# Performance work log

Hardware: AMD Instinct MI355X
Metric: run time of the kernel (lower is better)

Reference implementation:

```python
import jax, jax.numpy as jnp
import numpy as np

GROUPS = 8
EPS = 1e-5


def setup_inputs() -> dict:
    key = jax.random.key(0)
    ks = jax.random.split(key, 7)
    b, c, h, w = 32, 256, 32, 32
    x = jax.random.normal(ks[0], (b, c, h, w), dtype=jnp.float32)
    gn_weight = jax.random.normal(ks[1], (c,), dtype=jnp.float32) * 0.02 + 1.0
    gn_bias = jax.random.normal(ks[2], (c,), dtype=jnp.float32) * 0.02
    w_qkv = jax.random.normal(ks[3], (3 * c, c), dtype=jnp.float32) / np.sqrt(c)
    b_qkv = jax.random.normal(ks[4], (3 * c,), dtype=jnp.float32) * 0.01
    w_out = jax.random.normal(ks[5], (c, c), dtype=jnp.float32) / np.sqrt(c)
    b_out = jax.random.normal(ks[6], (c,), dtype=jnp.float32) * 0.01
    return {"x": x, "gn_weight": gn_weight, "gn_bias": gn_bias,
            "w_qkv": w_qkv, "b_qkv": b_qkv, "w_out": w_out, "b_out": b_out}


def group_norm(x, weight, bias):
    b, c, h, w = x.shape
    xg = x.reshape(b, GROUPS, c // GROUPS, h, w)
    mean = jnp.mean(xg, axis=(2, 3, 4), keepdims=True)
    var = jnp.var(xg, axis=(2, 3, 4), keepdims=True)
    xg = (xg - mean) * jax.lax.rsqrt(var + EPS)
    x = xg.reshape(b, c, h, w)
    return x * weight[None, :, None, None] + bias[None, :, None, None]


def reference(x, gn_weight, gn_bias, w_qkv, b_qkv, w_out, b_out):
    b, c, h, w = x.shape
    x_norm = group_norm(x, gn_weight, gn_bias)
    # 1x1 conv == channel matmul: (b, 3c, h, w)
    qkv = jnp.einsum('oc,bchw->bohw', w_qkv, x_norm) + b_qkv[None, :, None, None]
    q, k, v = jnp.split(qkv, 3, axis=1)
    hw = h * w
    q = q.reshape(b, c, hw)  # used transposed: (b, hw, c)
    k = k.reshape(b, c, hw)
    v = v.reshape(b, c, hw)
    scale = 1.0 / jnp.sqrt(jnp.float32(c))
    attn = jax.nn.softmax(jnp.einsum('bcs,bct->bst', q, k) * scale, axis=-1)  # (b, hw, hw)
    out = jnp.einsum('bst,bct->bcs', attn, v).reshape(b, c, h, w)
    out = jnp.einsum('oc,bchw->bohw', w_out, out) + b_out[None, :, None, None]
    return out + x
```

## Files before the change

### kernel.cpp

```cpp
#include <hip/hip_runtime.h>
#include <hip/hip_bf16.h>


typedef __bf16 bf16x8 __attribute__((ext_vector_type(8)));
typedef __bf16 bf16x4 __attribute__((ext_vector_type(4)));
typedef __bf16 bf16x2 __attribute__((ext_vector_type(2)));
typedef float f32x4 __attribute__((ext_vector_type(4)));
typedef float f32x16 __attribute__((ext_vector_type(16)));

#define MFMA16(a, b, c) __builtin_amdgcn_mfma_f32_16x16x32_bf16(a, b, c, 0, 0, 0)
#define MFMA32(a, b, c) __builtin_amdgcn_mfma_f32_32x32x16_bf16(a, b, c, 0, 0, 0)

__global__ __launch_bounds__(512) void gn_kernel(const float* __restrict__ x,
                                                 const float* __restrict__ gw,
                                                 const float* __restrict__ gb,
                                                 __bf16* __restrict__ xnT,
                                                 const float* __restrict__ wqkv,
                                                 const float* __restrict__ wout,
                                                 __bf16* __restrict__ wbf) {
    __shared__ float red[16];
    __shared__ float stats[2];
    __shared__ __bf16 Lds[512][40];
    const int b = blockIdx.x >> 3, g = blockIdx.x & 7;
    const size_t base = ((size_t)b * 256 + g * 32) * 1024;
    const float* xp = x + base;
    const int t = threadIdx.x;

    {
        int widx = (blockIdx.x * 512 + t) * 2;
        const float* wsrc = (widx < 196608) ? (wqkv + widx) : (wout + (widx - 196608));
        float2 wv = *(const float2*)wsrc;
        bf16x2 wo;
        wo[0] = (__bf16)wv.x; wo[1] = (__bf16)wv.y;
        *(bf16x2*)&wbf[widx] = wo;
    }

    float s = 0.f, s2 = 0.f;
    #pragma unroll
    for (int i = 0; i < 8; i++) {
        int j = i * 512 + t;
        float4 v0 = *(const float4*)(xp + (size_t)j * 8);
        float4 v1 = *(const float4*)(xp + (size_t)j * 8 + 4);
        s  += v0.x + v0.y + v0.z + v0.w + v1.x + v1.y + v1.z + v1.w;
        s2 += v0.x*v0.x + v0.y*v0.y + v0.z*v0.z + v0.w*v0.w
            + v1.x*v1.x + v1.y*v1.y + v1.z*v1.z + v1.w*v1.w;
    }
    #pragma unroll
    for (int o = 32; o > 0; o >>= 1) { s += __shfl_down(s, o, 64); s2 += __shfl_down(s2, o, 64); }
    const int wv = t >> 6;
    if ((t & 63) == 0) { red[wv * 2] = s; red[wv * 2 + 1] = s2; }
    __syncthreads();
    if (t == 0) {
        float ts = 0.f, ts2 = 0.f;
        for (int w = 0; w < 8; w++) { ts += red[w * 2]; ts2 += red[w * 2 + 1]; }
        float mean = ts / 32768.f;
        float var = ts2 / 32768.f - mean * mean;
        stats[0] = mean; stats[1] = rsqrtf(var + 1e-5f);
    }
    __syncthreads();
    const float mean = stats[0], inv = stats[1];

    const int c = t >> 4;
    const int so = (t & 15) * 2;
    const float ga = gw[g * 32 + c], be = gb[g * 32 + c];

    for (int chunk = 0; chunk < 1024; chunk += 512) {
        #pragma unroll
        for (int i = 0; i < 16; i++) {
            int sl = so + i * 32;
            float2 v = *(const float2*)(xp + (size_t)c * 1024 + chunk + sl);
            Lds[sl][c]     = (__bf16)((v.x - mean) * inv * ga + be);
            Lds[sl + 1][c] = (__bf16)((v.y - mean) * inv * ga + be);
        }
        __syncthreads();
        {
            int sl = t;
            #pragma unroll
            for (int u = 0; u < 4; u++) {
                bf16x8 vv = *(const bf16x8*)&Lds[sl][u * 8];
                *(bf16x8*)&xnT[((size_t)b * 1024 + chunk + sl) * 256 + g * 32 + u * 8] = vv;
            }
        }
        __syncthreads();
    }
}

#define GEMM64_BODY(ArowBase_, BrowBase_)                                               \
    f32x4 acc[4][4] = {};                                                               \
    const int r_ = t >> 1, kc_ = (t & 1) * 32;                                          \
    bf16x8 pa[4], pb[4];                                                                \
    _Pragma("unroll")                                                                   \
    for (int u = 0; u < 4; u++) {                                                       \
        pa[u] = *(const bf16x8*)&(ArowBase_)[(size_t)r_ * 256 + kc_ + u * 8];           \
        pb[u] = *(const bf16x8*)&(BrowBase_)[(size_t)r_ * 256 + kc_ + u * 8];           \
    }                                                                                   \
    for (int kk = 0; kk < 256; kk += 64) {                                              \
        _Pragma("unroll")                                                               \
        for (int u = 0; u < 4; u++) {                                                   \
            *(bf16x8*)&As[r_][kc_ + u * 8] = pa[u];                                     \
            *(bf16x8*)&Bs[r_][kc_ + u * 8] = pb[u];                                     \
        }                                                                               \
        __syncthreads();                                                                \
        if (kk < 192) {                                                                 \
            _Pragma("unroll")                                                           \
            for (int u = 0; u < 4; u++) {                                               \
                pa[u] = *(const bf16x8*)&(ArowBase_)[(size_t)r_ * 256 + kk + 64 + kc_ + u * 8]; \
                pb[u] = *(const bf16x8*)&(BrowBase_)[(size_t)r_ * 256 + kk + 64 + kc_ + u * 8]; \
            }                                                                           \
        }                                                                               \
        _Pragma("unroll")                                                               \
        for (int kh = 0; kh < 2; kh++) {                                                \
            bf16x8 af[4], bfv[4];                                                       \
            _Pragma("unroll")                                                           \
            for (int im = 0; im < 4; im++)                                              \
                af[im] = *(const bf16x8*)&As[wm + im * 16 + l16][kh * 32 + quad * 8];   \
            _Pragma("unroll")                                                           \
            for (int in = 0; in < 4; in++)                                              \
                bfv[in] = *(const bf16x8*)&Bs[wn + in * 16 + l16][kh * 32 + quad * 8];  \
            _Pragma("unroll")                                                           \
            for (int im = 0; im < 4; im++)                                              \
                _Pragma("unroll")                                                       \
                for (int in = 0; in < 4; in++)                                          \
                    acc[im][in] = MFMA16(af[im], bfv[in], acc[im][in]);                 \
        }                                                                               \
        __syncthreads();                                                                \
    }

__global__ __launch_bounds__(256) void qkv_gemm(const __bf16* __restrict__ wbf,
                                                const float* __restrict__ bias,
                                                const __bf16* __restrict__ xnT,
                                                __bf16* __restrict__ qtr,
                                                __bf16* __restrict__ ktr,
                                                __bf16* __restrict__ vbuf) {
    __shared__ union {
        struct { __bf16 A[128][72]; __bf16 B[128][72]; } g;
        __bf16 ct[128][136];
    } sm;
    const int b = blockIdx.z;
    const int n0 = blockIdx.x * 128, m0 = blockIdx.y * 128;
    const int t = threadIdx.x;
    const int wave = t >> 6, lane = t & 63, quad = lane >> 4, l16 = lane & 15;
    const int wm = (wave & 1) * 64, wn = (wave >> 1) * 64;
    const __bf16* arow = wbf + (size_t)m0 * 256;
    const __bf16* brow = xnT + ((size_t)b * 1024 + n0) * 256;
    auto As = sm.g.A;
    auto Bs = sm.g.B;

    GEMM64_BODY(arow, brow)

    if (m0 < 512) {
        #pragma unroll
        for (int im = 0; im < 4; im++) {
            #pragma unroll
            for (int in = 0; in < 4; in++) {
                int ob = m0 + wm + im * 16 + quad * 4;
                bf16x4 ov;
                #pragma unroll
                for (int r = 0; r < 4; r++) ov[r] = (__bf16)(acc[im][in][r] + bias[ob + r]);
                *(bf16x4*)&sm.ct[wn + in * 16 + l16][wm + im * 16 + quad * 4] = ov;
            }
        }
        __syncthreads();
        {
            const int rbase = t >> 2, cf = t & 3;
            #pragma unroll
            for (int rr = 0; rr < 2; rr++) {
                int row = rbase + rr * 64;
                int sg = n0 + row;
                __bf16* dst = (m0 < 256) ? &qtr[((size_t)b * 1024 + sg) * 256 + m0]
                                         : &ktr[((size_t)b * 1024 + sg) * 256 + (m0 - 256)];
                #pragma unroll
                for (int u = 0; u < 4; u++) {
                    int colb = cf * 8 + u * 32;
                    *(bf16x8*)&dst[colb] = *(const bf16x8*)&sm.ct[row][colb];
                }
            }
        }
    } else {
        #pragma unroll
        for (int im = 0; im < 4; im++) {
            #pragma unroll
            for (int in = 0; in < 4; in++) {
                int cl = wm + im * 16 + quad * 4;
                int tl = wn + in * 16 + l16;
                #pragma unroll
                for (int r = 0; r < 4; r++)
                    sm.ct[cl + r][tl] = (__bf16)(acc[im][in][r] + bias[m0 + cl + r]);
            }
        }
        __syncthreads();
        {
            const int row = t >> 1, tc = (t & 1) * 64;
            const int cglob = m0 - 512 + row;
            __bf16* dst = &vbuf[((size_t)b * 256 + cglob) * 1024 + n0 + tc];
            #pragma unroll
            for (int u = 0; u < 8; u++)
                *(bf16x8*)&dst[u * 8] = *(const bf16x8*)&sm.ct[row][tc + u * 8];
        }
    }
}

__global__ __launch_bounds__(512, 2) void attn_kernel(const __bf16* __restrict__ qtr,
                                                      const __bf16* __restrict__ ktr,
                                                      const __bf16* __restrict__ vbuf,
                                                      __bf16* __restrict__ aoT) {
    __shared__ __bf16 Kt[2][32][260];
    __shared__ __bf16 Vs[2][256][36];
    __shared__ bf16x8 Pl[4][2][2][64];
    __shared__ float Lred[4][2][32];
    const int b = blockIdx.x;
    const int tid = threadIdx.x;
    const int wave = tid >> 6, lane = tid & 63, half = lane >> 5, l31 = lane & 31;
    const int pair = wave & 3, th = wave >> 2;
    const int s0 = blockIdx.y * 128 + pair * 32;
    const float kscale = 0.09016844f;

    bf16x8 aq[16];
    #pragma unroll
    for (int ks = 0; ks < 16; ks++)
        aq[ks] = *(const bf16x8*)&qtr[((size_t)b * 1024 + s0 + l31) * 256 + ks * 16 + half * 8];

    const int k_row = tid >> 3;
    const int k_cb  = (tid & 7) * 8;
    const int v_c   = tid >> 1;
    const int v_th  = tid & 1;
    const size_t kbase = (size_t)b * 1024 * 256;
    const size_t vbase = (size_t)b * 256 * 1024;

    float l_acc = 0.f;
    f32x16 o_acc[4] = {};

    bf16x8 kpre[4], vpre[4];
    #pragma unroll
    for (int u = 0; u < 4; u++) {
        kpre[u] = *(const bf16x8*)&ktr[kbase + (size_t)k_row * 256 + k_cb + u * 64];
        vpre[u] = *(const bf16x8*)&vbuf[vbase + (size_t)v_c * 1024 + v_th * 32 + u * 8];
    }

    for (int it = 0; it < 16; it++) {
        #pragma unroll
        for (int u = 0; u < 4; u++)
            *(bf16x8*)&Kt[k_row >> 5][k_row & 31][k_cb + u * 64] = kpre[u];
        #pragma unroll
        for (int u = 0; u < 4; u++) {
            const bf16x4* hv = (const bf16x4*)&vpre[u];
            const int sbase = (u >> 1) * 16 + (u & 1) * 4;
            *(bf16x4*)&Vs[v_th][v_c][sbase]     = hv[0];
            *(bf16x4*)&Vs[v_th][v_c][sbase + 8] = hv[1];
        }
        __syncthreads();
        if (it < 15) {
            const int t1 = (it + 1) * 64;
            #pragma unroll
            for (int u = 0; u < 4; u++) {
                kpre[u] = *(const bf16x8*)&ktr[kbase + (size_t)(t1 + k_row) * 256 + k_cb + u * 64];
                vpre[u] = *(const bf16x8*)&vbuf[vbase + (size_t)v_c * 1024 + t1 + v_th * 32 + u * 8];
            }
        }

        f32x16 sc_a = {}, sc_b = {};
        __builtin_amdgcn_s_setprio(1);
        #pragma unroll
        for (int ks = 0; ks < 8; ks++) {
            bf16x8 bk0 = *(const bf16x8*)&Kt[th][l31][ks * 16 + half * 8];
            bf16x8 bk1 = *(const bf16x8*)&Kt[th][l31][(ks + 8) * 16 + half * 8];
            sc_a = MFMA32(bk0, aq[ks], sc_a);
            sc_b = MFMA32(bk1, aq[ks + 8], sc_b);
        }
        __builtin_amdgcn_s_setprio(0);

        bf16x8 pf0, pf1;
        #pragma unroll
        for (int r = 0; r < 8; r++) {
            float p = exp2f((sc_a[r] + sc_b[r]) * kscale);
            l_acc += p;
            pf0[r] = (__bf16)p;
        }
        #pragma unroll
        for (int r = 8; r < 16; r++) {
            float p = exp2f((sc_a[r] + sc_b[r]) * kscale);
            l_acc += p;
            pf1[r - 8] = (__bf16)p;
        }
        Pl[pair][th][0][lane] = pf0;
        Pl[pair][th][1][lane] = pf1;
        __syncthreads();
        bf16x8 pp0 = Pl[pair][1 - th][0][lane];
        bf16x8 pp1 = Pl[pair][1 - th][1][lane];

        bf16x8 ap[4];
        if (th == 0) { ap[0] = pf0; ap[1] = pf1; ap[2] = pp0; ap[3] = pp1; }
        else         { ap[0] = pp0; ap[1] = pp1; ap[2] = pf0; ap[3] = pf1; }

        __builtin_amdgcn_s_setprio(1);
        #pragma unroll
        for (int n = 0; n < 4; n++) {
            int c = th * 128 + n * 32 + l31;
            #pragma unroll
            for (int kc = 0; kc < 4; kc++) {
                bf16x8 bv = *(const bf16x8*)&Vs[kc >> 1][c][(kc & 1) * 16 + half * 8];
                o_acc[n] = MFMA32(ap[kc], bv, o_acc[n]);
            }
        }
        __builtin_amdgcn_s_setprio(0);
        __syncthreads();
    }

    l_acc += __shfl_xor(l_acc, 32, 64);
    if (lane < 32) Lred[pair][th][l31] = l_acc;
    __syncthreads();
    #pragma unroll
    for (int r = 0; r < 16; r++) {
        int row = (r & 3) + 8 * (r >> 2) + 4 * half;
        float rinv = 1.0f / (Lred[pair][0][row] + Lred[pair][1][row]);
        #pragma unroll
        for (int n = 0; n < 4; n++) {
            int c = th * 128 + n * 32 + l31;
            aoT[((size_t)b * 1024 + s0 + row) * 256 + c] = (__bf16)(o_acc[n][r] * rinv);
        }
    }
}

__global__ __launch_bounds__(256) void proj_gemm(const __bf16* __restrict__ wbf_out,
                                                 const float* __restrict__ bias,
                                                 const __bf16* __restrict__ aoT,
                                                 const float* __restrict__ resid,
                                                 float* __restrict__ Out) {
    __shared__ union {
        struct { __bf16 A[128][72]; __bf16 B[128][72]; } g;
        float cf[64][132];
    } sm;
    const int b = blockIdx.z;
    const int n0 = blockIdx.x * 128, m0 = blockIdx.y * 128;
    const int t = threadIdx.x;
    const int wave = t >> 6, lane = t & 63, quad = lane >> 4, l16 = lane & 15;
    const int wm = (wave & 1) * 64, wn = (wave >> 1) * 64;
    const __bf16* arow = wbf_out + (size_t)m0 * 256;
    const __bf16* brow = aoT + ((size_t)b * 1024 + n0) * 256;
    auto As = sm.g.A;
    auto Bs = sm.g.B;

    GEMM64_BODY(arow, brow)

    for (int h = 0; h < 2; h++) {
        if ((wave & 1) == h) {
            #pragma unroll
            for (int im = 0; im < 4; im++)
                #pragma unroll
                for (int in = 0; in < 4; in++)
                    #pragma unroll
                    for (int r = 0; r < 4; r++)
                        sm.cf[im * 16 + quad * 4 + r][wn + in * 16 + l16] = acc[im][in][r];
        }
        __syncthreads();
        {
            const int rloc = t >> 2, cq = (t & 3) * 4;
            const int o = m0 + h * 64 + rloc;
            const float bo = bias[o];
            const float* rrow = &resid[((size_t)b * 256 + o) * 1024 + n0];
            float* orow = &Out[((size_t)b * 256 + o) * 1024 + n0];
            #pragma unroll
            for (int u = 0; u < 8; u++) {
                int col = cq + u * 16;
                f32x4 cv = *(const f32x4*)&sm.cf[rloc][col];
                float4 rv = *(const float4*)&rrow[col];
                float4 ov;
                ov.x = cv[0] + bo + rv.x;
                ov.y = cv[1] + bo + rv.y;
                ov.z = cv[2] + bo + rv.z;
                ov.w = cv[3] + bo + rv.w;
                *(float4*)&orow[col] = ov;
            }
        }
        __syncthreads();
    }
}

extern "C" void kernel_launch(void* const* d_in, const int* in_sizes, int n_in,
                              void* d_out, int out_size, void* d_ws, size_t ws_size,
                              hipStream_t stream) {
    const float* x    = (const float*)d_in[0];
    const float* gw   = (const float*)d_in[1];
    const float* gb   = (const float*)d_in[2];
    const float* wqkv = (const float*)d_in[3];
    const float* bqkv = (const float*)d_in[4];
    const float* wout = (const float*)d_in[5];
    const float* bout = (const float*)d_in[6];
    float* out = (float*)d_out;

    const size_t T16 = (size_t)32 * 1024 * 256;
    __bf16* xnT  = (__bf16*)d_ws;
    __bf16* qtr  = xnT + T16;
    __bf16* ktr  = qtr + T16;
    __bf16* vbuf = ktr + T16;
    __bf16* aoT  = vbuf + T16;
    __bf16* wbf  = aoT + T16;

    gn_kernel<<<dim3(256), 512, 0, stream>>>(x, gw, gb, xnT, wqkv, wout, wbf);
    qkv_gemm<<<dim3(8, 6, 32), 256, 0, stream>>>(wbf, bqkv, xnT, qtr, ktr, vbuf);
    attn_kernel<<<dim3(32, 8), 512, 0, stream>>>(qtr, ktr, vbuf, aoT);
    proj_gemm<<<dim3(8, 2, 32), 256, 0, stream>>>(wbf + 196608, bout, aoT, x, out);
}
```

Measured before the change: 192.1 us.

## Double-buffer K/V tiles in LDS in attention kernel to drop a barrier

Doubles the shared-memory K and V staging buffers so the next tile is written to the alternate buffer while the current one is consumed. This removes the per-iteration barrier between staging and compute, and prefetches global loads two tiles ahead. The cost is roughly doubled LDS usage, which may cut resident blocks per CU and lower occupancy.

```diff
diff --git a/kernel.cpp b/kernel.cpp
--- a/kernel.cpp
+++ b/kernel.cpp
@@ -204,8 +204,8 @@
                                                       const __bf16* __restrict__ ktr,
                                                       const __bf16* __restrict__ vbuf,
                                                       __bf16* __restrict__ aoT) {
-    __shared__ __bf16 Kt[2][32][260];
-    __shared__ __bf16 Vs[2][256][36];
+    __shared__ __bf16 Kt[2][2][32][260];
+    __shared__ __bf16 Vs[2][2][256][36];
     __shared__ bf16x8 Pl[4][2][2][64];
     __shared__ float Lred[4][2][32];
     const int b = blockIdx.x;
@@ -229,41 +229,43 @@
 
     float l_acc = 0.f;
     f32x16 o_acc[4] = {};
-
     bf16x8 kpre[4], vpre[4];
-    #pragma unroll
-    for (int u = 0; u < 4; u++) {
-        kpre[u] = *(const bf16x8*)&ktr[kbase + (size_t)k_row * 256 + k_cb + u * 64];
-        vpre[u] = *(const bf16x8*)&vbuf[vbase + (size_t)v_c * 1024 + v_th * 32 + u * 8];
-    }
+
+#define LOAD_KV(T_)                                                                           \
+    _Pragma("unroll")                                                                         \
+    for (int u = 0; u < 4; u++) {                                                             \
+        kpre[u] = *(const bf16x8*)&ktr[kbase + (size_t)((T_) + k_row) * 256 + k_cb + u * 64]; \
+        vpre[u] = *(const bf16x8*)&vbuf[vbase + (size_t)v_c * 1024 + (T_) + v_th * 32 + u * 8]; \
+    }
+
+#define STAGE_KV(bb_)                                                                         \
+    _Pragma("unroll")                                                                         \
+    for (int u = 0; u < 4; u++)                                                               \
+        *(bf16x8*)&Kt[bb_][k_row >> 5][k_row & 31][k_cb + u * 64] = kpre[u];                  \
+    _Pragma("unroll")                                                                         \
+    for (int u = 0; u < 4; u++) {                                                             \
+        const bf16x4* hv = (const bf16x4*)&vpre[u];                                           \
+        const int sbase = (u >> 1) * 16 + (u & 1) * 4;                                        \
+        *(bf16x4*)&Vs[bb_][v_th][v_c][sbase]     = hv[0];                                     \
+        *(bf16x4*)&Vs[bb_][v_th][v_c][sbase + 8] = hv[1];                                     \
+    }
+
+    LOAD_KV(0)
+    STAGE_KV(0)
+    LOAD_KV(64)
+    __syncthreads();
 
     for (int it = 0; it < 16; it++) {
-        #pragma unroll
-        for (int u = 0; u < 4; u++)
-            *(bf16x8*)&Kt[k_row >> 5][k_row & 31][k_cb + u * 64] = kpre[u];
-        #pragma unroll
-        for (int u = 0; u < 4; u++) {
-            const bf16x4* hv = (const bf16x4*)&vpre[u];
-            const int sbase = (u >> 1) * 16 + (u & 1) * 4;
-            *(bf16x4*)&Vs[v_th][v_c][sbase]     = hv[0];
-            *(bf16x4*)&Vs[v_th][v_c][sbase + 8] = hv[1];
-        }
-        __syncthreads();
-        if (it < 15) {
-            const int t1 = (it + 1) * 64;
-            #pragma unroll
-            for (int u = 0; u < 4; u++) {
-                kpre[u] = *(const bf16x8*)&ktr[kbase + (size_t)(t1 + k_row) * 256 + k_cb + u * 64];
-                vpre[u] = *(const bf16x8*)&vbuf[vbase + (size_t)v_c * 1024 + t1 + v_th * 32 + u * 8];
-            }
-        }
+        const int cur = it & 1;
+        if (it < 15) { STAGE_KV(cur ^ 1) }
+        if (it < 14) { LOAD_KV((it + 2) * 64) }
 
         f32x16 sc_a = {}, sc_b = {};
         __builtin_amdgcn_s_setprio(1);
         #pragma unroll
         for (int ks = 0; ks < 8; ks++) {
-            bf16x8 bk0 = *(const bf16x8*)&Kt[th][l31][ks * 16 + half * 8];
-            bf16x8 bk1 = *(const bf16x8*)&Kt[th][l31][(ks + 8) * 16 + half * 8];
+            bf16x8 bk0 = *(const bf16x8*)&Kt[cur][th][l31][ks * 16 + half * 8];
+            bf16x8 bk1 = *(const bf16x8*)&Kt[cur][th][l31][(ks + 8) * 16 + half * 8];
             sc_a = MFMA32(bk0, aq[ks], sc_a);
             sc_b = MFMA32(bk1, aq[ks + 8], sc_b);
         }
@@ -298,13 +300,15 @@
             int c = th * 128 + n * 32 + l31;
             #pragma unroll
             for (int kc = 0; kc < 4; kc++) {
-                bf16x8 bv = *(const bf16x8*)&Vs[kc >> 1][c][(kc & 1) * 16 + half * 8];
+                bf16x8 bv = *(const bf16x8*)&Vs[cur][kc >> 1][c][(kc & 1) * 16 + half * 8];
                 o_acc[n] = MFMA32(ap[kc], bv, o_acc[n]);
             }
         }
         __builtin_amdgcn_s_setprio(0);
         __syncthreads();
     }
+#undef LOAD_KV
+#undef STAGE_KV
 
     l_acc += __shfl_xor(l_acc, 32, 64);
     if (lane < 32) Lred[pair][th][l31] = l_acc;
```

Measured after the change: 195.9 us. Within noise of the previous version (+2.0%).

## Load GEMM tiles directly into LDS with global_load_lds and XOR swizzle

Applied to the files above, without the earlier changes.

Replaces the register-staged global-to-LDS copy in the QKV and output projection GEMMs with direct global_load_lds transfers of 16 bytes per lane. The padded LDS rows become unpadded and use an XOR swizzle on the 8-element column chunk to avoid bank conflicts. The aim is to cut VGPR pressure and the extra LDS store instructions. In exchange it drops the register prefetch of the next K slice, so loads are no longer overlapped with the MFMA work.

```diff
diff --git a/kernel.cpp b/kernel.cpp
--- a/kernel.cpp
+++ b/kernel.cpp
@@ -10,6 +10,10 @@
 
 #define MFMA16(a, b, c) __builtin_amdgcn_mfma_f32_16x16x32_bf16(a, b, c, 0, 0, 0)
 #define MFMA32(a, b, c) __builtin_amdgcn_mfma_f32_32x32x16_bf16(a, b, c, 0, 0, 0)
+
+#define GLD16(gsrc_, ldst_)                                                                  \
+    __builtin_amdgcn_global_load_lds((const __attribute__((address_space(1))) void*)(gsrc_), \
+                                     (__attribute__((address_space(3))) void*)(ldst_), 16, 0, 0)
 
 __global__ __launch_bounds__(512) void gn_kernel(const float* __restrict__ x,
                                                  const float* __restrict__ gw,
@@ -85,38 +89,31 @@
     }
 }
 
-#define GEMM64_BODY(ArowBase_, BrowBase_)                                               \
+#define GEMM64G_BODY(ArowBase_, BrowBase_)                                              \
     f32x4 acc[4][4] = {};                                                               \
-    const int r_ = t >> 1, kc_ = (t & 1) * 32;                                          \
-    bf16x8 pa[4], pb[4];                                                                \
-    _Pragma("unroll")                                                                   \
-    for (int u = 0; u < 4; u++) {                                                       \
-        pa[u] = *(const bf16x8*)&(ArowBase_)[(size_t)r_ * 256 + kc_ + u * 8];           \
-        pb[u] = *(const bf16x8*)&(BrowBase_)[(size_t)r_ * 256 + kc_ + u * 8];           \
-    }                                                                                   \
     for (int kk = 0; kk < 256; kk += 64) {                                              \
         _Pragma("unroll")                                                               \
-        for (int u = 0; u < 4; u++) {                                                   \
-            *(bf16x8*)&As[r_][kc_ + u * 8] = pa[u];                                     \
-            *(bf16x8*)&Bs[r_][kc_ + u * 8] = pb[u];                                     \
+        for (int i = 0; i < 4; i++) {                                                   \
+            const int ch = wave * 4 + i;                                                \
+            const int r = ch * 8 + (lane >> 3);                                         \
+            const int sw = ((lane & 7) ^ (r & 7)) * 8;                                  \
+            GLD16((ArowBase_) + (size_t)r * 256 + kk + sw, (char*)&As[0][0] + ch * 1024); \
+            GLD16((BrowBase_) + (size_t)r * 256 + kk + sw, (char*)&Bs[0][0] + ch * 1024); \
         }                                                                               \
         __syncthreads();                                                                \
-        if (kk < 192) {                                                                 \
-            _Pragma("unroll")                                                           \
-            for (int u = 0; u < 4; u++) {                                               \
-                pa[u] = *(const bf16x8*)&(ArowBase_)[(size_t)r_ * 256 + kk + 64 + kc_ + u * 8]; \
-                pb[u] = *(const bf16x8*)&(BrowBase_)[(size_t)r_ * 256 + kk + 64 + kc_ + u * 8]; \
-            }                                                                           \
-        }                                                                               \
         _Pragma("unroll")                                                               \
         for (int kh = 0; kh < 2; kh++) {                                                \
             bf16x8 af[4], bfv[4];                                                       \
             _Pragma("unroll")                                                           \
-            for (int im = 0; im < 4; im++)                                              \
-                af[im] = *(const bf16x8*)&As[wm + im * 16 + l16][kh * 32 + quad * 8];   \
+            for (int im = 0; im < 4; im++) {                                            \
+                const int row = wm + im * 16 + l16;                                     \
+                af[im] = *(const bf16x8*)&As[row][(((kh * 4 + quad) ^ (row & 7)) * 8)]; \
+            }                                                                           \
             _Pragma("unroll")                                                           \
-            for (int in = 0; in < 4; in++)                                              \
-                bfv[in] = *(const bf16x8*)&Bs[wn + in * 16 + l16][kh * 32 + quad * 8];  \
+            for (int in = 0; in < 4; in++) {                                            \
+                const int row = wn + in * 16 + l16;                                     \
+                bfv[in] = *(const bf16x8*)&Bs[row][(((kh * 4 + quad) ^ (row & 7)) * 8)]; \
+            }                                                                           \
             _Pragma("unroll")                                                           \
             for (int im = 0; im < 4; im++)                                              \
                 _Pragma("unroll")                                                       \
@@ -133,7 +130,7 @@
                                                 __bf16* __restrict__ ktr,
                                                 __bf16* __restrict__ vbuf) {
     __shared__ union {
-        struct { __bf16 A[128][72]; __bf16 B[128][72]; } g;
+        struct { __bf16 A[128][64]; __bf16 B[128][64]; } g;
         __bf16 ct[128][136];
     } sm;
     const int b = blockIdx.z;
@@ -146,7 +143,7 @@
     auto As = sm.g.A;
     auto Bs = sm.g.B;
 
-    GEMM64_BODY(arow, brow)
+    GEMM64G_BODY(arow, brow)
 
     if (m0 < 512) {
         #pragma unroll
@@ -327,7 +324,7 @@
                                                  const float* __restrict__ resid,
                                                  float* __restrict__ Out) {
     __shared__ union {
-        struct { __bf16 A[128][72]; __bf16 B[128][72]; } g;
+        struct { __bf16 A[128][64]; __bf16 B[128][64]; } g;
         float cf[64][132];
     } sm;
     const int b = blockIdx.z;
@@ -340,7 +337,7 @@
     auto As = sm.g.A;
     auto Bs = sm.g.B;
 
-    GEMM64_BODY(arow, brow)
+    GEMM64G_BODY(arow, brow)
 
     for (int h = 0; h < 2; h++) {
         if ((wave & 1) == h) {
```

After: 190.7 us. Within noise of the previous version (-0.7%).
